# Kernel tuning notes

Hardware: AMD Instinct MI355X
Metric: run time of the kernel (lower is better)

## Reference

```python
import jax, jax.numpy as jnp
import numpy as np

N_NODES = 50000
N_EDGES = 800000
IN_F, HID, OUT_F = 256, 128, 64
ATTN_SLOPE = 0.2   # DGL GATConv negative_slope default
ACT_SLOPE = 0.01   # nn.LeakyReLU default


def setup_inputs() -> dict:
    key = jax.random.key(0)
    ks = jax.random.split(key, 7)
    x = jax.random.normal(ks[0], (N_NODES, IN_F), dtype=jnp.float32)
    src = jax.random.randint(ks[1], (N_EDGES,), 0, N_NODES, dtype=jnp.int32)
    dst = jax.random.randint(ks[2], (N_EDGES,), 0, N_NODES, dtype=jnp.int32)
    W_gat = jax.random.normal(ks[3], (IN_F, HID), dtype=jnp.float32) * (1.0 / np.sqrt(IN_F))
    attn_l = jax.random.normal(ks[4], (HID,), dtype=jnp.float32) * 0.1
    attn_r = jax.random.normal(ks[5], (HID,), dtype=jnp.float32) * 0.1
    bias_gat = jnp.zeros((HID,), dtype=jnp.float32)
    W_lin = jax.random.normal(ks[6], (OUT_F, HID), dtype=jnp.float32) * (1.0 / np.sqrt(HID))
    return {"x": x, "src": src, "dst": dst, "W_gat": W_gat, "attn_l": attn_l,
            "attn_r": attn_r, "bias_gat": bias_gat, "W_lin": W_lin}


def reference(x, src, dst, W_gat, attn_l, attn_r, bias_gat, W_lin):
    N = x.shape[0]
    # GATConv (num_heads=1): linear projection then additive attention
    feat = x @ W_gat                         # [N, HID]
    el = feat @ attn_l                        # [N]  (sum(feat * a_l, -1))
    er = feat @ attn_r                        # [N]
    # per-edge logits, leaky_relu(0.2)
    e = jax.nn.leaky_relu(el[src] + er[dst], negative_slope=ATTN_SLOPE)  # [E]
    # segment softmax over edges grouped by destination node
    e_max = jax.ops.segment_max(e, dst, num_segments=N)  # [N] (-inf for isolated)
    alpha = jnp.exp(e - e_max[dst])                      # [E]
    denom = jax.ops.segment_sum(alpha, dst, num_segments=N)
    a = alpha / denom[dst]                               # [E]
    # scatter-weighted aggregation of source features
    msg = a[:, None] * feat[src]                         # [E, HID]
    agg = jax.ops.segment_sum(msg, dst, num_segments=N) + bias_gat  # [N, HID]
    # outer wrapper: LeakyReLU(0.01), squeeze (head dim already gone), linear no bias
    gene = jax.nn.leaky_relu(agg, negative_slope=ACT_SLOPE)
    return gene @ W_lin.T                                # [N, OUT_F]
```

## Files before the change

### kernel.cpp

```cpp
#include <hip/hip_runtime.h>
#include <hip/hip_bf16.h>


#define NNODES 50000
#define NEDGES 800000
#define IN_F   256
#define HID    128
#define OUTF   64

#define PA_EPT   8
#define PA_EDGES (256 * PA_EPT)
#define PA_NB    ((NEDGES + PA_EDGES - 1) / PA_EDGES)
#define NBKT     ((NNODES + 255) / 256)
#define BCAP     5120
#define NSTRIP   (NNODES / 16)
#define GB       ((NSTRIP + 3) / 4)

#define AGN      16
#define AGSLOT   64
#define AGB      3136

typedef unsigned short u16;
typedef unsigned long long u64;
typedef __bf16 bf16x8 __attribute__((ext_vector_type(8)));
typedef float  f32x4  __attribute__((ext_vector_type(4)));

__device__ __forceinline__ u16 f2b(float f) {
    union { float f; unsigned u; } v; v.f = f;
    unsigned u = v.u;
    return (u16)((u + 0x7fffu + ((u >> 16) & 1u)) >> 16);
}
__device__ __forceinline__ float b2f_lo(unsigned v) {
    union { unsigned u; float f; } c; c.u = (v & 0xffffu) << 16; return c.f;
}
__device__ __forceinline__ float b2f_hi(unsigned v) {
    union { unsigned u; float f; } c; c.u = v & 0xffff0000u; return c.f;
}
__device__ __forceinline__ float lrelu02_exp(float t) {
    t = t > 0.f ? t : 0.2f * t;
    return __expf(t);
}

__global__ __launch_bounds__(256) void pack0(const float* __restrict__ Wg,
                                             const float* __restrict__ Wl,
                                             u16* __restrict__ pWg,
                                             u16* __restrict__ pWl,
                                             int* __restrict__ bcnt) {
    int blk = blockIdx.x, tid = threadIdx.x;
    if (blk < 16) {
        int t = blk * 256 + tid;
        int lane = t & 63, tile = t >> 6;
        int nt = tile & 7, kt = tile >> 3;
        int col = lane & 15, quad = lane >> 4;
        int krow = kt * 32 + quad * 8;
        int ncol = nt * 16 + col;
#pragma unroll
        for (int j = 0; j < 8; j++) pWg[t * 8 + j] = f2b(Wg[(krow + j) * HID + ncol]);
    } else if (blk < 20) {
        int t = (blk - 16) * 256 + tid;
        int lane = t & 63, tile = t >> 6;
        int nt = tile & 3, kt = tile >> 2;
        int col = lane & 15, quad = lane >> 4;
        int o  = nt * 16 + col;
        int k0 = kt * 32 + quad * 8;
#pragma unroll
        for (int j = 0; j < 8; j++) pWl[t * 8 + j] = f2b(Wl[o * HID + k0 + j]);
    } else {
        if (tid < NBKT) bcnt[tid] = 0;
    }
}

__global__ __launch_bounds__(256) void k_mega(
        const float* __restrict__ x, const u16* __restrict__ pWg,
        const float* __restrict__ al_, const float* __restrict__ ar_,
        unsigned* __restrict__ feat2, float* __restrict__ el, float* __restrict__ er,
        const int* __restrict__ src, const int* __restrict__ dst,
        int* __restrict__ bcnt, u64* __restrict__ pairs) {
    __shared__ u64 smemU[21504 / 8];
    char* smem = (char*)smemU;
    int blk = blockIdx.x, tid = threadIdx.x;

    if (blk < GB) {
        int wave = tid >> 6, lane = tid & 63;
        int strip = blk * 4 + wave;
        if (strip >= NSTRIP) return;
        int m0 = strip * 16;
        int col = lane & 15, quad = lane >> 4;

        f32x4 xa[16];
        const float* xr = x + (size_t)(m0 + col) * IN_F + quad * 8;
#pragma unroll
        for (int kt = 0; kt < 8; kt++) {
            xa[2 * kt]     = *reinterpret_cast<const f32x4*>(xr + kt * 32);
            xa[2 * kt + 1] = *reinterpret_cast<const f32x4*>(xr + kt * 32 + 4);
        }
        bf16x8 av[8];
#pragma unroll
        for (int kt = 0; kt < 8; kt++)
#pragma unroll
            for (int j = 0; j < 4; j++) {
                av[kt][j]     = (__bf16)xa[2 * kt][j];
                av[kt][4 + j] = (__bf16)xa[2 * kt + 1][j];
            }

        f32x4 acc[8] = {};
#pragma unroll
        for (int kt = 0; kt < 8; kt++)
#pragma unroll
            for (int nt = 0; nt < 8; nt++) {
                bf16x8 b = *reinterpret_cast<const bf16x8*>(pWg + ((kt * 8 + nt) * 64 + lane) * 8);
                acc[nt] = __builtin_amdgcn_mfma_f32_16x16x32_bf16(av[kt], b, acc[nt], 0, 0, 0);
            }

        float pl[4] = {0, 0, 0, 0}, pr[4] = {0, 0, 0, 0};
#pragma unroll
        for (int nt = 0; nt < 8; nt++) {
            float alv = al_[nt * 16 + col], arv = ar_[nt * 16 + col];
#pragma unroll
            for (int reg = 0; reg < 4; reg++) {
                pl[reg] += acc[nt][reg] * alv;
                pr[reg] += acc[nt][reg] * arv;
            }
        }
#pragma unroll
        for (int m = 1; m < 16; m <<= 1)
#pragma unroll
            for (int reg = 0; reg < 4; reg++) {
                pl[reg] += __shfl_xor(pl[reg], m, 64);
                pr[reg] += __shfl_xor(pr[reg], m, 64);
            }
        if (col == 0) {
#pragma unroll
            for (int reg = 0; reg < 4; reg++) {
                el[m0 + quad * 4 + reg] = pl[reg];
                er[m0 + quad * 4 + reg] = pr[reg];
            }
        }
#pragma unroll
        for (int nt = 0; nt < 8; nt++)
#pragma unroll
            for (int reg = 0; reg < 4; reg++) {
                u16* fp = (u16*)feat2;
                fp[(size_t)(m0 + quad * 4 + reg) * HID + nt * 16 + col] = f2b(acc[nt][reg]);
            }
        return;
    }

    int* hist    = (int*)smem;
    int* binbase = hist + 256;
    int* gbase   = binbase + 256;
    int* fill    = gbase + 256;
    int* stmp    = fill + 256;
    u64* spair   = (u64*)(smem + 5120);

    int e0 = (blk - GB) * PA_EDGES;
    int cnt = NEDGES - e0; if (cnt > PA_EDGES) cnt = PA_EDGES;

    hist[tid] = 0; fill[tid] = 0;
    __syncthreads();

    int es[PA_EPT], ed[PA_EPT];
#pragma unroll
    for (int j = 0; j < PA_EPT; j++) {
        int idx = e0 + j * 256 + tid;
        if (idx < NEDGES) {
            es[j] = src[idx];
            ed[j] = dst[idx];
            atomicAdd(&hist[ed[j] >> 8], 1);
        } else ed[j] = -1;
    }
    __syncthreads();

    stmp[tid] = (tid < NBKT) ? hist[tid] : 0;
    __syncthreads();
#pragma unroll
    for (int ofs = 1; ofs < 256; ofs <<= 1) {
        int u = (tid >= ofs) ? stmp[tid - ofs] : 0;
        __syncthreads();
        stmp[tid] += u;
        __syncthreads();
    }
    if (tid < NBKT) {
        binbase[tid] = stmp[tid] - hist[tid];
        if (hist[tid] > 0)
            gbase[tid] = tid * BCAP + atomicAdd(&bcnt[tid], hist[tid]);
    }
    __syncthreads();

#pragma unroll
    for (int j = 0; j < PA_EPT; j++) {
        if (ed[j] >= 0) {
            int b = ed[j] >> 8;
            int r = atomicAdd(&fill[b], 1);
            int loc = binbase[b] + r;
            spair[loc] = ((u64)(unsigned)ed[j] << 32) | (unsigned)es[j];
        }
    }
    __syncthreads();

    for (int i = tid; i < cnt; i += 256) {
        u64 p = spair[i];
        int b = (int)(p >> 40);
        pairs[gbase[b] + (i - binbase[b])] = p;
    }
}

__global__ __launch_bounds__(256) void k_aggslim(const u64* __restrict__ pairs,
                                                 const int* __restrict__ bcnt,
                                                 const float* __restrict__ el,
                                                 const float* __restrict__ er,
                                                 const unsigned* __restrict__ feat2,
                                                 const float* __restrict__ bias,
                                                 const u16* __restrict__ pWl,
                                                 float* __restrict__ out) {
    __shared__ int   cnt_l[AGN];
    __shared__ float erl[AGN];
    __shared__ int   ssrc[AGN * AGSLOT];
    __shared__ float swgt[AGN * AGSLOT];
    __shared__ unsigned sg[AGN * 68];

    int tid = threadIdx.x;
    int wave = tid >> 6, lane = tid & 63;
    int logical = (blockIdx.x & 7) * 392 + (blockIdx.x >> 3);
    int nb = logical * AGN;
    if (nb >= NNODES) return;
    int cb = logical >> 4;

    if (tid < AGN) {
        cnt_l[tid] = 0;
        erl[tid] = er[nb + tid];
    }
    __syncthreads();

    int cntb = bcnt[cb];
    const u64* reg = pairs + (size_t)cb * BCAP;
    for (int i = tid; i < cntb; i += 256) {
        u64 p = reg[i];
        int d = (int)(unsigned)(p >> 32);
        unsigned dl = (unsigned)(d - nb);
        if (dl < (unsigned)AGN) {
            int s = (int)(unsigned)(p & 0xffffffffu);
            float w = lrelu02_exp(el[s] + erl[dl]);
            int slot = atomicAdd(&cnt_l[dl], 1);
            if (slot < AGSLOT) {
                ssrc[dl * AGSLOT + slot] = s;
                swgt[dl * AGSLOT + slot] = w;
            }
        }
    }
    __syncthreads();

    float bl = bias[lane * 2 + 0], bh = bias[lane * 2 + 1];
    for (int i = 0; i < 4; i++) {
        int dl = wave * 4 + i;
        int cnt = cnt_l[dl]; if (cnt > AGSLOT) cnt = AGSLOT;
        const int*   ep = ssrc + dl * AGSLOT;
        const float* wp = swgt + dl * AGSLOT;

        float p0 = 0.f, p1 = 0.f, q0 = 0.f, q1 = 0.f;
        float r0 = 0.f, r1 = 0.f, t0 = 0.f, t1 = 0.f;
        float u0 = 0.f, u1 = 0.f, x0 = 0.f, x1 = 0.f;
        float y0 = 0.f, y1 = 0.f, z0 = 0.f, z1 = 0.f;
        float dn = 0.f;
        int j = 0;
        for (; j + 8 <= cnt; j += 8) {
            int4 sa = *reinterpret_cast<const int4*>(ep + j);
            int4 sb = *reinterpret_cast<const int4*>(ep + j + 4);
            float4 wa = *reinterpret_cast<const float4*>(wp + j);
            float4 wb = *reinterpret_cast<const float4*>(wp + j + 4);
            unsigned v0 = feat2[(size_t)sa.x * 64 + lane];
            unsigned v1 = feat2[(size_t)sa.y * 64 + lane];
            unsigned v2 = feat2[(size_t)sa.z * 64 + lane];
            unsigned v3 = feat2[(size_t)sa.w * 64 + lane];
            unsigned v4 = feat2[(size_t)sb.x * 64 + lane];
            unsigned v5 = feat2[(size_t)sb.y * 64 + lane];
            unsigned v6 = feat2[(size_t)sb.z * 64 + lane];
            unsigned v7 = feat2[(size_t)sb.w * 64 + lane];
            p0 += wa.x * b2f_lo(v0); p1 += wa.x * b2f_hi(v0);
            q0 += wa.y * b2f_lo(v1); q1 += wa.y * b2f_hi(v1);
            r0 += wa.z * b2f_lo(v2); r1 += wa.z * b2f_hi(v2);
            t0 += wa.w * b2f_lo(v3); t1 += wa.w * b2f_hi(v3);
            u0 += wb.x * b2f_lo(v4); u1 += wb.x * b2f_hi(v4);
            x0 += wb.y * b2f_lo(v5); x1 += wb.y * b2f_hi(v5);
            y0 += wb.z * b2f_lo(v6); y1 += wb.z * b2f_hi(v6);
            z0 += wb.w * b2f_lo(v7); z1 += wb.w * b2f_hi(v7);
            dn += ((wa.x + wa.y) + (wa.z + wa.w)) + ((wb.x + wb.y) + (wb.z + wb.w));
        }
        if (j + 4 <= cnt) {
            int4 sa = *reinterpret_cast<const int4*>(ep + j);
            float4 wa = *reinterpret_cast<const float4*>(wp + j);
            unsigned v0 = feat2[(size_t)sa.x * 64 + lane];
            unsigned v1 = feat2[(size_t)sa.y * 64 + lane];
            unsigned v2 = feat2[(size_t)sa.z * 64 + lane];
            unsigned v3 = feat2[(size_t)sa.w * 64 + lane];
            p0 += wa.x * b2f_lo(v0); p1 += wa.x * b2f_hi(v0);
            q0 += wa.y * b2f_lo(v1); q1 += wa.y * b2f_hi(v1);
            r0 += wa.z * b2f_lo(v2); r1 += wa.z * b2f_hi(v2);
            t0 += wa.w * b2f_lo(v3); t1 += wa.w * b2f_hi(v3);
            dn += (wa.x + wa.y) + (wa.z + wa.w);
            j += 4;
        }
        for (; j < cnt; j++) {
            int s = ep[j];
            float w = wp[j];
            unsigned v = feat2[(size_t)s * 64 + lane];
            p0 += w * b2f_lo(v); p1 += w * b2f_hi(v);
            dn += w;
        }
        float a0 = ((p0 + q0) + (r0 + t0)) + ((u0 + x0) + (y0 + z0));
        float a1 = ((p1 + q1) + (r1 + t1)) + ((u1 + x1) + (y1 + z1));

        float inv = dn > 0.f ? 1.f / dn : 0.f;
        float g0 = a0 * inv + bl;
        float g1 = a1 * inv + bh;
        g0 = g0 > 0.f ? g0 : 0.01f * g0;
        g1 = g1 > 0.f ? g1 : 0.01f * g1;
        sg[(wave * 4 + i) * 68 + lane] = (unsigned)f2b(g0) | ((unsigned)f2b(g1) << 16);
    }
    __syncthreads();

    int col = lane & 15, quad = lane >> 4;
    int nt = wave;
    f32x4 acc = {};
#pragma unroll
    for (int kt = 0; kt < 4; kt++) {
        bf16x8 a = *reinterpret_cast<const bf16x8*>(&sg[col * 68 + kt * 16 + quad * 4]);
        bf16x8 bf = *reinterpret_cast<const bf16x8*>(pWl + ((kt * 4 + nt) * 64 + lane) * 8);
        acc = __builtin_amdgcn_mfma_f32_16x16x32_bf16(a, bf, acc, 0, 0, 0);
    }
#pragma unroll
    for (int reg = 0; reg < 4; reg++)
        out[(size_t)(nb + quad * 4 + reg) * OUTF + nt * 16 + col] = acc[reg];
}

extern "C" void kernel_launch(void* const* d_in, const int* in_sizes, int n_in,
                              void* d_out, int out_size, void* d_ws, size_t ws_size,
                              hipStream_t stream) {
    const float* x      = (const float*)d_in[0];
    const int*   src    = (const int*)d_in[1];
    const int*   dst    = (const int*)d_in[2];
    const float* Wg     = (const float*)d_in[3];
    const float* attn_l = (const float*)d_in[4];
    const float* attn_r = (const float*)d_in[5];
    const float* bias   = (const float*)d_in[6];
    const float* Wl     = (const float*)d_in[7];
    float* out          = (float*)d_out;

    char* ws = (char*)d_ws;
    size_t off = 0;
    auto alloc = [&](size_t b) { size_t r = off; off += (b + 255) & ~(size_t)255; return r; };
    size_t pwgOff  = alloc((size_t)8 * 8 * 64 * 8 * 2);
    size_t pwlOff  = alloc((size_t)4 * 4 * 64 * 8 * 2);
    size_t featOff = alloc((size_t)NNODES * HID * 2);
    size_t elOff   = alloc((size_t)NNODES * 4);
    size_t erOff   = alloc((size_t)NNODES * 4);
    size_t pairOff = alloc((size_t)NBKT * BCAP * 8);
    size_t bcntOff = alloc((size_t)NBKT * 4);

    u16*      pWg   = (u16*)(ws + pwgOff);
    u16*      pWl   = (u16*)(ws + pwlOff);
    unsigned* feat2 = (unsigned*)(ws + featOff);
    float*    el    = (float*)(ws + elOff);
    float*    er    = (float*)(ws + erOff);
    u64*      pairs = (u64*)(ws + pairOff);
    int*      bcnt  = (int*)(ws + bcntOff);

    pack0<<<21, 256, 0, stream>>>(Wg, Wl, pWg, pWl, bcnt);
    k_mega<<<GB + PA_NB, 256, 0, stream>>>(x, pWg, attn_l, attn_r, feat2, el, er,
                                           src, dst, bcnt, pairs);
    k_aggslim<<<AGB, 256, 0, stream>>>(pairs, bcnt, el, er, feat2, bias,
                                       pWl, out);
}
```

Before: 165.1 us.

## Shrink destination buckets from 256 to 64 nodes for edge partitioning

Edges are now binned into buckets of 64 destination nodes instead of 256, with a 4-bins-per-thread scan in the partition pass and a smaller per-bucket capacity. Each aggregation block handling 16 nodes now scans a bucket about a quarter the size, so far fewer irrelevant pairs are read and filtered. In exchange the partition pass uses more shared memory and does more global atomics per block. BCAP 1536 leaves headroom over the expected 1024 edges per bucket, but an overflow would corrupt results.

```diff
diff --git a/kernel.cpp b/kernel.cpp
--- a/kernel.cpp
+++ b/kernel.cpp
@@ -11,8 +11,8 @@
 #define PA_EPT   8
 #define PA_EDGES (256 * PA_EPT)
 #define PA_NB    ((NEDGES + PA_EDGES - 1) / PA_EDGES)
-#define NBKT     ((NNODES + 255) / 256)
-#define BCAP     5120
+#define NBKT     ((NNODES + 63) / 64)
+#define BCAP     1536
 #define NSTRIP   (NNODES / 16)
 #define GB       ((NSTRIP + 3) / 4)
 
@@ -66,7 +66,7 @@
 #pragma unroll
         for (int j = 0; j < 8; j++) pWl[t * 8 + j] = f2b(Wl[o * HID + k0 + j]);
     } else {
-        if (tid < NBKT) bcnt[tid] = 0;
+        for (int i = tid; i < NBKT; i += 256) bcnt[i] = 0;
     }
 }
 
@@ -76,7 +76,7 @@
         unsigned* __restrict__ feat2, float* __restrict__ el, float* __restrict__ er,
         const int* __restrict__ src, const int* __restrict__ dst,
         int* __restrict__ bcnt, u64* __restrict__ pairs) {
-    __shared__ u64 smemU[21504 / 8];
+    __shared__ u64 smemU[33792 / 8];
     char* smem = (char*)smemU;
     int blk = blockIdx.x, tid = threadIdx.x;
 
@@ -146,17 +146,17 @@
         return;
     }
 
-    int* hist    = (int*)smem;
-    int* binbase = hist + 256;
-    int* gbase   = binbase + 256;
-    int* fill    = gbase + 256;
-    int* stmp    = fill + 256;
-    u64* spair   = (u64*)(smem + 5120);
+    int* hist  = (int*)smem;
+    int* bbase = hist + 1024;
+    int* gb    = bbase + 1024;
+    int* fill  = gb + 1024;
+    int* pt    = fill + 1024;
+    u64* spair = (u64*)(smem + 17408);
 
     int e0 = (blk - GB) * PA_EDGES;
     int cnt = NEDGES - e0; if (cnt > PA_EDGES) cnt = PA_EDGES;
 
-    hist[tid] = 0; fill[tid] = 0;
+    for (int i = tid; i < 1024; i += 256) { hist[i] = 0; fill[i] = 0; }
     __syncthreads();
 
     int es[PA_EPT], ed[PA_EPT];
@@ -166,33 +166,40 @@
         if (idx < NEDGES) {
             es[j] = src[idx];
             ed[j] = dst[idx];
-            atomicAdd(&hist[ed[j] >> 8], 1);
+            atomicAdd(&hist[ed[j] >> 6], 1);
         } else ed[j] = -1;
     }
     __syncthreads();
 
-    stmp[tid] = (tid < NBKT) ? hist[tid] : 0;
+    int b0 = 4 * tid;
+    int h0 = hist[b0], h1 = hist[b0 + 1], h2 = hist[b0 + 2], h3 = hist[b0 + 3];
+    int tt = h0 + h1 + h2 + h3;
+    pt[tid] = tt;
     __syncthreads();
 #pragma unroll
     for (int ofs = 1; ofs < 256; ofs <<= 1) {
-        int u = (tid >= ofs) ? stmp[tid - ofs] : 0;
+        int u = (tid >= ofs) ? pt[tid - ofs] : 0;
         __syncthreads();
-        stmp[tid] += u;
+        pt[tid] += u;
         __syncthreads();
     }
-    if (tid < NBKT) {
-        binbase[tid] = stmp[tid] - hist[tid];
-        if (hist[tid] > 0)
-            gbase[tid] = tid * BCAP + atomicAdd(&bcnt[tid], hist[tid]);
-    }
+    int ex = pt[tid] - tt;
+    bbase[b0]     = ex;
+    bbase[b0 + 1] = ex + h0;
+    bbase[b0 + 2] = ex + h0 + h1;
+    bbase[b0 + 3] = ex + h0 + h1 + h2;
+    if (h0 > 0) gb[b0]     = b0 * BCAP       + atomicAdd(&bcnt[b0], h0);
+    if (h1 > 0) gb[b0 + 1] = (b0 + 1) * BCAP + atomicAdd(&bcnt[b0 + 1], h1);
+    if (h2 > 0) gb[b0 + 2] = (b0 + 2) * BCAP + atomicAdd(&bcnt[b0 + 2], h2);
+    if (h3 > 0) gb[b0 + 3] = (b0 + 3) * BCAP + atomicAdd(&bcnt[b0 + 3], h3);
     __syncthreads();
 
 #pragma unroll
     for (int j = 0; j < PA_EPT; j++) {
         if (ed[j] >= 0) {
-            int b = ed[j] >> 8;
+            int b = ed[j] >> 6;
             int r = atomicAdd(&fill[b], 1);
-            int loc = binbase[b] + r;
+            int loc = bbase[b] + r;
             spair[loc] = ((u64)(unsigned)ed[j] << 32) | (unsigned)es[j];
         }
     }
@@ -200,8 +207,8 @@
 
     for (int i = tid; i < cnt; i += 256) {
         u64 p = spair[i];
-        int b = (int)(p >> 40);
-        pairs[gbase[b] + (i - binbase[b])] = p;
+        int b = (int)(p >> 38);
+        pairs[gb[b] + (i - bbase[b])] = p;
     }
 }
 
@@ -224,7 +231,7 @@
     int logical = (blockIdx.x & 7) * 392 + (blockIdx.x >> 3);
     int nb = logical * AGN;
     if (nb >= NNODES) return;
-    int cb = logical >> 4;
+    int cb = logical >> 2;
 
     if (tid < AGN) {
         cnt_l[tid] = 0;
```

After: 171.1 us. 3.6% more time.

## Gather 16-byte feature rows across 4 edge groups per wave and shuffle-reduce

Applied to the files above, without the earlier changes.

Restructures the per-destination aggregation so each wave splits its 64 lanes into 4 edge groups of 16 lanes. Each lane loads 16 bytes (8 bf16 features) per edge instead of 4 bytes, and the partial sums are combined with cross-lane xor shuffles. Source index and weight are packed into one u64 in shared memory, zero-filled so padded slots add nothing. The softmax denominator is now accumulated with a shared-memory atomic during binning. The aim is fewer, wider global gather instructions and less loop overhead, at the cost of extra LDS atomics, a zero-fill pass and shuffle reductions.

```diff
diff --git a/kernel.cpp b/kernel.cpp
--- a/kernel.cpp
+++ b/kernel.cpp
@@ -214,9 +214,9 @@
                                                  const u16* __restrict__ pWl,
                                                  float* __restrict__ out) {
     __shared__ int   cnt_l[AGN];
+    __shared__ float dls[AGN];
     __shared__ float erl[AGN];
-    __shared__ int   ssrc[AGN * AGSLOT];
-    __shared__ float swgt[AGN * AGSLOT];
+    __shared__ u64   sws[AGN * AGSLOT];
     __shared__ unsigned sg[AGN * 68];
 
     int tid = threadIdx.x;
@@ -228,8 +228,10 @@
 
     if (tid < AGN) {
         cnt_l[tid] = 0;
+        dls[tid] = 0.f;
         erl[tid] = er[nb + tid];
     }
+    for (int i = tid; i < AGN * AGSLOT; i += 256) sws[i] = 0ull;
     __syncthreads();
 
     int cntb = bcnt[cb];
@@ -241,81 +243,74 @@
         if (dl < (unsigned)AGN) {
             int s = (int)(unsigned)(p & 0xffffffffu);
             float w = lrelu02_exp(el[s] + erl[dl]);
+            atomicAdd(&dls[dl], w);
             int slot = atomicAdd(&cnt_l[dl], 1);
             if (slot < AGSLOT) {
-                ssrc[dl * AGSLOT + slot] = s;
-                swgt[dl * AGSLOT + slot] = w;
-            }
-        }
-    }
-    __syncthreads();
-
-    float bl = bias[lane * 2 + 0], bh = bias[lane * 2 + 1];
+                union { float f; unsigned u; } wu; wu.f = w;
+                sws[dl * AGSLOT + slot] = ((u64)wu.u << 32) | (unsigned)s;
+            }
+        }
+    }
+    __syncthreads();
+
+    int fl = lane & 15;
+    int eg = lane >> 4;
+    f32x4 bA = *reinterpret_cast<const f32x4*>(bias + fl * 8);
+    f32x4 bB = *reinterpret_cast<const f32x4*>(bias + fl * 8 + 4);
+
     for (int i = 0; i < 4; i++) {
         int dl = wave * 4 + i;
         int cnt = cnt_l[dl]; if (cnt > AGSLOT) cnt = AGSLOT;
-        const int*   ep = ssrc + dl * AGSLOT;
-        const float* wp = swgt + dl * AGSLOT;
-
-        float p0 = 0.f, p1 = 0.f, q0 = 0.f, q1 = 0.f;
-        float r0 = 0.f, r1 = 0.f, t0 = 0.f, t1 = 0.f;
-        float u0 = 0.f, u1 = 0.f, x0 = 0.f, x1 = 0.f;
-        float y0 = 0.f, y1 = 0.f, z0 = 0.f, z1 = 0.f;
-        float dn = 0.f;
-        int j = 0;
-        for (; j + 8 <= cnt; j += 8) {
-            int4 sa = *reinterpret_cast<const int4*>(ep + j);
-            int4 sb = *reinterpret_cast<const int4*>(ep + j + 4);
-            float4 wa = *reinterpret_cast<const float4*>(wp + j);
-            float4 wb = *reinterpret_cast<const float4*>(wp + j + 4);
-            unsigned v0 = feat2[(size_t)sa.x * 64 + lane];
-            unsigned v1 = feat2[(size_t)sa.y * 64 + lane];
-            unsigned v2 = feat2[(size_t)sa.z * 64 + lane];
-            unsigned v3 = feat2[(size_t)sa.w * 64 + lane];
-            unsigned v4 = feat2[(size_t)sb.x * 64 + lane];
-            unsigned v5 = feat2[(size_t)sb.y * 64 + lane];
-            unsigned v6 = feat2[(size_t)sb.z * 64 + lane];
-            unsigned v7 = feat2[(size_t)sb.w * 64 + lane];
-            p0 += wa.x * b2f_lo(v0); p1 += wa.x * b2f_hi(v0);
-            q0 += wa.y * b2f_lo(v1); q1 += wa.y * b2f_hi(v1);
-            r0 += wa.z * b2f_lo(v2); r1 += wa.z * b2f_hi(v2);
-            t0 += wa.w * b2f_lo(v3); t1 += wa.w * b2f_hi(v3);
-            u0 += wb.x * b2f_lo(v4); u1 += wb.x * b2f_hi(v4);
-            x0 += wb.y * b2f_lo(v5); x1 += wb.y * b2f_hi(v5);
-            y0 += wb.z * b2f_lo(v6); y1 += wb.z * b2f_hi(v6);
-            z0 += wb.w * b2f_lo(v7); z1 += wb.w * b2f_hi(v7);
-            dn += ((wa.x + wa.y) + (wa.z + wa.w)) + ((wb.x + wb.y) + (wb.z + wb.w));
-        }
-        if (j + 4 <= cnt) {
-            int4 sa = *reinterpret_cast<const int4*>(ep + j);
-            float4 wa = *reinterpret_cast<const float4*>(wp + j);
-            unsigned v0 = feat2[(size_t)sa.x * 64 + lane];
-            unsigned v1 = feat2[(size_t)sa.y * 64 + lane];
-            unsigned v2 = feat2[(size_t)sa.z * 64 + lane];
-            unsigned v3 = feat2[(size_t)sa.w * 64 + lane];
-            p0 += wa.x * b2f_lo(v0); p1 += wa.x * b2f_hi(v0);
-            q0 += wa.y * b2f_lo(v1); q1 += wa.y * b2f_hi(v1);
-            r0 += wa.z * b2f_lo(v2); r1 += wa.z * b2f_hi(v2);
-            t0 += wa.w * b2f_lo(v3); t1 += wa.w * b2f_hi(v3);
-            dn += (wa.x + wa.y) + (wa.z + wa.w);
-            j += 4;
-        }
-        for (; j < cnt; j++) {
-            int s = ep[j];
-            float w = wp[j];
-            unsigned v = feat2[(size_t)s * 64 + lane];
-            p0 += w * b2f_lo(v); p1 += w * b2f_hi(v);
-            dn += w;
-        }
-        float a0 = ((p0 + q0) + (r0 + t0)) + ((u0 + x0) + (y0 + z0));
-        float a1 = ((p1 + q1) + (r1 + t1)) + ((u1 + x1) + (y1 + z1));
-
-        float inv = dn > 0.f ? 1.f / dn : 0.f;
-        float g0 = a0 * inv + bl;
-        float g1 = a1 * inv + bh;
-        g0 = g0 > 0.f ? g0 : 0.01f * g0;
-        g1 = g1 > 0.f ? g1 : 0.01f * g1;
-        sg[(wave * 4 + i) * 68 + lane] = (unsigned)f2b(g0) | ((unsigned)f2b(g1) << 16);
+        int ng = (cnt + 7) >> 3;
+        const u64* swp = sws + dl * AGSLOT + eg;
+
+        float a0 = 0.f, a1 = 0.f, a2 = 0.f, a3 = 0.f;
+        float a4 = 0.f, a5 = 0.f, a6 = 0.f, a7 = 0.f;
+        for (int j = 0; j < ng; j++) {
+            u64 ws0 = swp[j * 8];
+            u64 ws1 = swp[j * 8 + 4];
+            int s0 = (int)(unsigned)(ws0 & 0xffffffffu);
+            int s1 = (int)(unsigned)(ws1 & 0xffffffffu);
+            union { unsigned u; float f; } w0c, w1c;
+            w0c.u = (unsigned)(ws0 >> 32);
+            w1c.u = (unsigned)(ws1 >> 32);
+            float w0 = w0c.f, w1 = w1c.f;
+            uint4 v0 = *reinterpret_cast<const uint4*>(feat2 + ((size_t)s0 << 6) + fl * 4);
+            uint4 v1 = *reinterpret_cast<const uint4*>(feat2 + ((size_t)s1 << 6) + fl * 4);
+            a0 += w0 * b2f_lo(v0.x); a1 += w0 * b2f_hi(v0.x);
+            a2 += w0 * b2f_lo(v0.y); a3 += w0 * b2f_hi(v0.y);
+            a4 += w0 * b2f_lo(v0.z); a5 += w0 * b2f_hi(v0.z);
+            a6 += w0 * b2f_lo(v0.w); a7 += w0 * b2f_hi(v0.w);
+            a0 += w1 * b2f_lo(v1.x); a1 += w1 * b2f_hi(v1.x);
+            a2 += w1 * b2f_lo(v1.y); a3 += w1 * b2f_hi(v1.y);
+            a4 += w1 * b2f_lo(v1.z); a5 += w1 * b2f_hi(v1.z);
+            a6 += w1 * b2f_lo(v1.w); a7 += w1 * b2f_hi(v1.w);
+        }
+        a0 += __shfl_xor(a0, 16, 64); a1 += __shfl_xor(a1, 16, 64);
+        a2 += __shfl_xor(a2, 16, 64); a3 += __shfl_xor(a3, 16, 64);
+        a4 += __shfl_xor(a4, 16, 64); a5 += __shfl_xor(a5, 16, 64);
+        a6 += __shfl_xor(a6, 16, 64); a7 += __shfl_xor(a7, 16, 64);
+        a0 += __shfl_xor(a0, 32, 64); a1 += __shfl_xor(a1, 32, 64);
+        a2 += __shfl_xor(a2, 32, 64); a3 += __shfl_xor(a3, 32, 64);
+        a4 += __shfl_xor(a4, 32, 64); a5 += __shfl_xor(a5, 32, 64);
+        a6 += __shfl_xor(a6, 32, 64); a7 += __shfl_xor(a7, 32, 64);
+
+        float dnv = dls[dl];
+        float inv = dnv > 0.f ? 1.f / dnv : 0.f;
+        float g0 = a0 * inv + bA[0], g1 = a1 * inv + bA[1];
+        float g2 = a2 * inv + bA[2], g3 = a3 * inv + bA[3];
+        float g4 = a4 * inv + bB[0], g5 = a5 * inv + bB[1];
+        float g6 = a6 * inv + bB[2], g7 = a7 * inv + bB[3];
+        g0 = g0 > 0.f ? g0 : 0.01f * g0; g1 = g1 > 0.f ? g1 : 0.01f * g1;
+        g2 = g2 > 0.f ? g2 : 0.01f * g2; g3 = g3 > 0.f ? g3 : 0.01f * g3;
+        g4 = g4 > 0.f ? g4 : 0.01f * g4; g5 = g5 > 0.f ? g5 : 0.01f * g5;
+        g6 = g6 > 0.f ? g6 : 0.01f * g6; g7 = g7 > 0.f ? g7 : 0.01f * g7;
+        if (eg == 0) {
+            sg[dl * 68 + fl * 4 + 0] = (unsigned)f2b(g0) | ((unsigned)f2b(g1) << 16);
+            sg[dl * 68 + fl * 4 + 1] = (unsigned)f2b(g2) | ((unsigned)f2b(g3) << 16);
+            sg[dl * 68 + fl * 4 + 2] = (unsigned)f2b(g4) | ((unsigned)f2b(g5) << 16);
+            sg[dl * 68 + fl * 4 + 3] = (unsigned)f2b(g6) | ((unsigned)f2b(g7) << 16);
+        }
     }
     __syncthreads();
 
```

New measurement: 167.6 us. About the same (+1.5%).
